# Kernel optimization log

Measured on AMD Instinct MI355X. Metric: run time of the kernel, lower is better.

## Reference

```python
import jax, jax.numpy as jnp
import numpy as np

D_MODEL = 1024
NHEAD = 16
HEAD_DIM = D_MODEL // NHEAD


def setup_inputs() -> dict:
    key = jax.random.key(0)
    ks = jax.random.split(key, 11)
    B, S = 2, 2048
    scale = 1.0 / np.sqrt(D_MODEL)
    inp = {
        "query": jax.random.normal(ks[0], (B, S, D_MODEL), jnp.float32),
        "key": jax.random.normal(ks[1], (B, S, D_MODEL), jnp.float32),
        "value": jax.random.normal(ks[2], (B, S, D_MODEL), jnp.float32),
        "Wq": jax.random.normal(ks[3], (D_MODEL, D_MODEL), jnp.float32) * scale,
        "bq": jnp.zeros((D_MODEL,), jnp.float32),
        "Wk": jax.random.normal(ks[4], (D_MODEL, D_MODEL), jnp.float32) * scale,
        "bk": jnp.zeros((D_MODEL,), jnp.float32),
        "Wv": jax.random.normal(ks[5], (D_MODEL, D_MODEL), jnp.float32) * scale,
        "bv": jnp.zeros((D_MODEL,), jnp.float32),
        "Wo": jax.random.normal(ks[6], (D_MODEL, D_MODEL), jnp.float32) * scale,
        "bo": jnp.zeros((D_MODEL,), jnp.float32),
    }
    return inp


def reference(query, key, value, Wq, bq, Wk, bk, Wv, bv, Wo, bo):
    B, S, _ = query.shape
    # Linear projections (torch Linear: x @ W.T + b)
    def proj(x, W, b):
        y = x @ W.T + b
        return y.reshape(B, -1, NHEAD, HEAD_DIM).transpose(0, 2, 1, 3)  # [B,H,S,hd]
    q = proj(query, Wq, bq)
    k = proj(key, Wk, bk)
    v = proj(value, Wv, bv)
    scores = jnp.einsum("bhqd,bhkd->bhqk", q, k) / np.sqrt(HEAD_DIM)
    attn = jax.nn.softmax(scores, axis=-1)  # dropout is identity (eval / p=0)
    out = jnp.einsum("bhqk,bhkd->bhqd", attn, v)
    out = out.transpose(0, 2, 1, 3).reshape(B, S, D_MODEL)
    return out @ Wo.T + bo
```

## Files before the change

### kernel.cpp

```cpp
#include <hip/hip_runtime.h>
#include <stdint.h>

typedef __attribute__((ext_vector_type(8))) short bf16x8;
typedef __attribute__((ext_vector_type(4))) short bf16x4;
typedef __attribute__((ext_vector_type(4))) float f32x4;
typedef __attribute__((ext_vector_type(2))) unsigned int u32x2;
typedef __attribute__((ext_vector_type(4))) unsigned int u32x4;
typedef unsigned int u32;
typedef unsigned short u16;

#define S_LEN 2048
#define DMODEL 1024
#define HD 64


static __device__ __forceinline__ u16 f2bf(float f) {
  u32 u = __builtin_bit_cast(u32, f);
  return (u16)((u + 0x7fffu + ((u >> 16) & 1u)) >> 16);
}

static __device__ __forceinline__ u32 cvt_pk(float a, float b) {
  u32 r;
  asm("v_cvt_pk_bf16_f32 %0, %1, %2" : "=v"(r) : "v"(a), "v"(b));
  return r;
}

static __device__ __forceinline__ void gl_lds16(const u16* g, u16* l) {
  __builtin_amdgcn_global_load_lds((const __attribute__((address_space(1))) u32*)g,
                                   (__attribute__((address_space(3))) u32*)l, 16, 0, 0);
}

static __device__ __forceinline__ u32 lds_addr(const void* p) {
  return (u32)(uint64_t)p;
}

static __device__ __forceinline__ bf16x4 tr16(u32 addr) {
  bf16x4 r;
  asm volatile("ds_read_b64_tr_b16 %0, %1" : "=v"(r) : "v"(addr));
  return r;
}

__global__ __launch_bounds__(256) void convert_w(
    const float* __restrict__ wq, const float* __restrict__ wk,
    const float* __restrict__ wv, const float* __restrict__ wo,
    u16* __restrict__ dst) {
  size_t i = ((size_t)blockIdx.x * 256 + threadIdx.x) * 8;
  u32 wsel = (u32)((i >> 20) & 3u);
  const float* src = (wsel == 0) ? wq : (wsel == 1) ? wk : (wsel == 2) ? wv : wo;
  size_t off = i & 0xFFFFFu;
  float4 a = *(const float4*)(src + off);
  float4 b = *(const float4*)(src + off + 4);
  bf16x8 o;
  o[0] = (short)f2bf(a.x); o[1] = (short)f2bf(a.y);
  o[2] = (short)f2bf(a.z); o[3] = (short)f2bf(a.w);
  o[4] = (short)f2bf(b.x); o[5] = (short)f2bf(b.y);
  o[6] = (short)f2bf(b.z); o[7] = (short)f2bf(b.w);
  *(bf16x8*)(dst + i) = o;
}

template <int OUT_BF16, int BN>
static __device__ __forceinline__ void gemm_core(
    const u16* __restrict__ A, const u16* __restrict__ Bm,
    const float* __restrict__ bias, void* __restrict__ Y, float scale,
    int bm, int bn, u16* As, u16* Bs) {
  const int tid = threadIdx.x;
  const int lane = tid & 63, w = tid >> 6;
  const int wm = w >> 1, wn = w & 1;
  const int g = lane >> 4, l15 = lane & 15;
  constexpr int NFR = BN / 64 * 2;

  f32x4 acc[4][NFR] = {};

  const int r0 = tid >> 2, k8 = (tid & 3) * 8;
  const int r1 = (tid + 256) >> 2;
  const size_t arow0 = (size_t)(bm * 128 + r0) * DMODEL + k8;
  const size_t arow1 = (size_t)(bm * 128 + r1) * DMODEL + k8;
  const size_t brow0 = (size_t)(bn * BN + r0) * DMODEL + k8;
  const size_t brow1 = (size_t)(bn * BN + r1) * DMODEL + k8;

  auto stage = [&](int buf, int kt) {
    const int kb = kt * 32;
    u16* asb = As + buf * 4096;
    u16* bsb = Bs + buf * (BN * 32);
    gl_lds16(A + arow0 + kb, asb + w * 512);
    gl_lds16(A + arow1 + kb, asb + w * 512 + 2048);
    gl_lds16(Bm + brow0 + kb, bsb + w * 512);
    if constexpr (BN == 128) gl_lds16(Bm + brow1 + kb, bsb + w * 512 + 2048);
  };

  stage(0, 0);
  __syncthreads();
  int cur = 0;
  for (int kt = 0; kt < 32; ++kt) {
    if (kt < 31) stage(cur ^ 1, kt + 1);
    const u16* as = As + cur * 4096;
    const u16* bs = Bs + cur * (BN * 32);
    bf16x8 a[4], b[NFR];
#pragma unroll
    for (int mi = 0; mi < 4; ++mi)
      a[mi] = *(const bf16x8*)&as[(wm * 64 + mi * 16 + l15) * 32 + g * 8];
#pragma unroll
    for (int ni = 0; ni < NFR; ++ni)
      b[ni] = *(const bf16x8*)&bs[(wn * (BN / 2) + ni * 16 + l15) * 32 + g * 8];
#pragma unroll
    for (int mi = 0; mi < 4; ++mi)
#pragma unroll
      for (int ni = 0; ni < NFR; ++ni)
        acc[mi][ni] = __builtin_amdgcn_mfma_f32_16x16x32_bf16(a[mi], b[ni], acc[mi][ni], 0, 0, 0);
    __syncthreads();
    cur ^= 1;
  }

#pragma unroll
  for (int ni = 0; ni < NFR; ++ni) {
    const int col = bn * BN + wn * (BN / 2) + ni * 16 + l15;
    const float bv = bias[col];
#pragma unroll
    for (int mi = 0; mi < 4; ++mi) {
      const int row0 = bm * 128 + wm * 64 + mi * 16 + g * 4;
#pragma unroll
      for (int r = 0; r < 4; ++r) {
        float v = (acc[mi][ni][r] + bv) * scale;
        if (OUT_BF16)
          ((u16*)Y)[(size_t)(row0 + r) * DMODEL + col] = f2bf(v);
        else
          ((float*)Y)[(size_t)(row0 + r) * DMODEL + col] = v;
      }
    }
  }
}

__global__ __launch_bounds__(512, 6) void qkv_gemm(
    const float* __restrict__ xq, const float* __restrict__ xk, const float* __restrict__ xv,
    const u16* __restrict__ W,
    const float* __restrict__ bq, const float* __restrict__ bk, const float* __restrict__ bv,
    u16* __restrict__ Qp, u16* __restrict__ Kpp, u16* __restrict__ Vpp, float qscale) {
  __shared__ u16 As[2 * 4096];
  __shared__ u16 Bs[2 * 4096];
  const int sel = blockIdx.x >> 8;
  const int bb = blockIdx.x & 255;
  const int bm = (bb & 7) * 4 + (bb >> 6);
  const int bn = (bb >> 3) & 7;
  const float* A = (sel == 0) ? xq : (sel == 1) ? xk : xv;
  const u16* Bm = W + (size_t)sel * (1024 * 1024);
  const float* bias = (sel == 0) ? bq : (sel == 1) ? bk : bv;
  u16* Y = (sel == 0) ? Qp : (sel == 1) ? Kpp : Vpp;
  const float scale = (sel == 0) ? qscale : 1.0f;

  const int tid = threadIdx.x;
  const int lane = tid & 63, w = tid >> 6;
  const int wm = w >> 2, wn = w & 3;
  const int g = lane >> 4, l15 = lane & 15;

  f32x4 acc[4][2] = {};

  const int r0 = tid >> 2, k8 = (tid & 3) * 8;
  const size_t arow0 = (size_t)(bm * 128 + r0) * DMODEL + k8;
  const size_t brow0 = (size_t)(bn * 128 + r0) * DMODEL + k8;

  float4 af0, af1;
  auto loadA = [&](int kt) {
    const int kb = kt * 32;
    af0 = *(const float4*)(A + arow0 + kb);
    af1 = *(const float4*)(A + arow0 + kb + 4);
  };
  auto writeA = [&](int buf) {
    u16* asb = As + buf * 4096;
    u32x4 p0 = {cvt_pk(af0.x, af0.y), cvt_pk(af0.z, af0.w),
                cvt_pk(af1.x, af1.y), cvt_pk(af1.z, af1.w)};
    *(u32x4*)(asb + tid * 8) = p0;
  };
  auto stageB = [&](int buf, int kt) {
    const int kb = kt * 32;
    u16* bsb = Bs + buf * 4096;
    gl_lds16(Bm + brow0 + kb, bsb + w * 512);
  };

  loadA(0);
  stageB(0, 0);
  writeA(0);
  __syncthreads();
  int cur = 0;
  for (int kt = 0; kt < 32; ++kt) {
    if (kt < 31) {
      loadA(kt + 1);
      stageB(cur ^ 1, kt + 1);
    }
    const u16* as = As + cur * 4096;
    const u16* bs = Bs + cur * 4096;
    bf16x8 a[4], b[2];
#pragma unroll
    for (int mi = 0; mi < 4; ++mi)
      a[mi] = *(const bf16x8*)&as[(wm * 64 + mi * 16 + l15) * 32 + g * 8];
#pragma unroll
    for (int ni = 0; ni < 2; ++ni)
      b[ni] = *(const bf16x8*)&bs[(wn * 32 + ni * 16 + l15) * 32 + g * 8];
#pragma unroll
    for (int mi = 0; mi < 4; ++mi)
#pragma unroll
      for (int ni = 0; ni < 2; ++ni)
        acc[mi][ni] = __builtin_amdgcn_mfma_f32_16x16x32_bf16(a[mi], b[ni], acc[mi][ni], 0, 0, 0);
    if (kt < 31) writeA(cur ^ 1);
    __syncthreads();
    cur ^= 1;
  }

#pragma unroll
  for (int ni = 0; ni < 2; ++ni) {
    const int col = bn * 128 + wn * 32 + ni * 16 + l15;
    const float bv = bias[col];
#pragma unroll
    for (int mi = 0; mi < 4; ++mi) {
      const int row0 = bm * 128 + wm * 64 + mi * 16 + g * 4;
#pragma unroll
      for (int r = 0; r < 4; ++r) {
        float v = (acc[mi][ni][r] + bv) * scale;
        ((u16*)Y)[(size_t)(row0 + r) * DMODEL + col] = f2bf(v);
      }
    }
  }
}

__global__ __launch_bounds__(256) void wo_gemm(
    const u16* __restrict__ A, const u16* __restrict__ Bm,
    const float* __restrict__ bias, float* __restrict__ Y) {
  __shared__ u16 As[2 * 4096];
  __shared__ u16 Bs[2 * 2048];
  const int idx = blockIdx.x;
  const int bm = (idx & 7) * 4 + (idx >> 7);
  const int bn = (idx >> 3) & 15;
  gemm_core<0, 64>(A, Bm, bias, Y, 1.0f, bm, bn, As, Bs);
}

__global__ __launch_bounds__(512, 4) void attn_fwd(
    const u16* __restrict__ Qp, const u16* __restrict__ Kp,
    const u16* __restrict__ Vp, u16* __restrict__ Op) {
  __shared__ u16 smem[32768];
  u16* Kl = smem;
  u16* Vl = smem + 8192;
  const int tid = threadIdx.x;
  const int lane = tid & 63, w = tid >> 6;
  const int g = lane >> 4, l15 = lane & 15;
  const int qs = w & 3, hf = w >> 2;
  const int xcd = blockIdx.x & 7;
  const int idx = blockIdx.x >> 3;
  const int bh = xcd * 4 + (idx >> 4);
  const int qt = idx & 15;
  const int b = bh >> 4, h = bh & 15;
  const size_t rowbase = (size_t)b * S_LEN;
  const int hcol = h * HD;

  bf16x8 qf[2][2];
#pragma unroll
  for (int qb = 0; qb < 2; ++qb) {
    const int qrow = qt * 128 + qs * 32 + qb * 16 + l15;
    qf[qb][0] = *(const bf16x8*)(Qp + (rowbase + qrow) * DMODEL + hcol + g * 8);
    qf[qb][1] = *(const bf16x8*)(Qp + (rowbase + qrow) * DMODEL + hcol + 32 + g * 8);
  }

  f32x4 o[2][4] = {};
  float lsum[2] = {0.0f, 0.0f};

  const u32 sbase = lds_addr(smem);

  const int half_s = tid >> 8;
  const int kvs = (tid >> 3) & 31, slot = (tid & 7) ^ (kvs & 7);
  const size_t koff = (rowbase + half_s * 1024 + kvs) * (size_t)DMODEL + hcol + slot * 8;
  const int cc = tid & 255;
  const int hh = cc & 1, p = (cc >> 1) & 15, sub = (cc >> 5) & 1, dt0 = (cc >> 6) & 3;
  const int kvv = 8 * (p >> 2) + sub * 4 + (p & 3);
  const size_t voff = (rowbase + half_s * 1024 + kvv) * (size_t)DMODEL + hcol + dt0 * 16 + hh * 8;

  auto stage = [&](int buf, int it) {
    const size_t adv = (size_t)it * 32 * DMODEL;
    gl_lds16(Kp + koff + adv, Kl + buf * 4096 + w * 512);
    gl_lds16(Vp + voff + adv, Vl + buf * 4096 + w * 512);
  };

  stage(0, 0);
  __syncthreads();
  int cur = 0;
  for (int it = 0; it < 32; ++it) {
    if (it < 31) stage(cur ^ 1, it + 1);
    const char* kb = (const char*)smem + cur * 8192 + hf * 4096;
    const u32 vbb = sbase + 16384 + (u32)(cur * 8192 + hf * 4096);
    const u32 pswz = (u32)((l15 & 7) << 4);

    f32x4 s[2][2];
    __builtin_amdgcn_s_setprio(1);
#pragma unroll
    for (int t = 0; t < 2; ++t) {
      const int kvl = t * 16 + l15;
      const u32 swz = (u32)((kvl & 7) << 4);
      bf16x8 k0 = *(const bf16x8*)(kb + (((u32)(kvl * 128 + g * 16)) ^ swz));
      bf16x8 k1 = *(const bf16x8*)(kb + (((u32)(kvl * 128 + 64 + g * 16)) ^ swz));
      f32x4 z = {};
      s[0][t] = __builtin_amdgcn_mfma_f32_16x16x32_bf16(
          k1, qf[0][1], __builtin_amdgcn_mfma_f32_16x16x32_bf16(k0, qf[0][0], z, 0, 0, 0), 0, 0, 0);
      s[1][t] = __builtin_amdgcn_mfma_f32_16x16x32_bf16(
          k1, qf[1][1], __builtin_amdgcn_mfma_f32_16x16x32_bf16(k0, qf[1][0], z, 0, 0, 0), 0, 0, 0);
    }
    __builtin_amdgcn_s_setprio(0);

#pragma unroll
    for (int qb = 0; qb < 2; ++qb) {
      const u32 pb = (u32)(32768 + (w * 2 + qb) * 2048 + l15 * 128);
      float psum = 0.0f;
#pragma unroll
      for (int t = 0; t < 2; ++t) {
        float e0 = __builtin_amdgcn_exp2f(s[qb][t][0]);
        float e1 = __builtin_amdgcn_exp2f(s[qb][t][1]);
        float e2 = __builtin_amdgcn_exp2f(s[qb][t][2]);
        float e3 = __builtin_amdgcn_exp2f(s[qb][t][3]);
        psum += (e0 + e1) + (e2 + e3);
        u32x2 pk = {cvt_pk(e0, e1), cvt_pk(e2, e3)};
        *(u32x2*)((char*)smem + ((pb + (u32)(t * 32 + g * 8)) ^ pswz)) = pk;
      }
      lsum[qb] += psum;
    }

    bf16x8 pf[2];
    bf16x4 tv[4][2];
#pragma unroll
    for (int qb = 0; qb < 2; ++qb) {
      const u32 pb = (u32)(32768 + (w * 2 + qb) * 2048 + l15 * 128);
      pf[qb] = *(const bf16x8*)((const char*)smem + ((pb + (u32)(g * 16)) ^ pswz));
    }
#pragma unroll
    for (int dt = 0; dt < 4; ++dt)
#pragma unroll
      for (int sb = 0; sb < 2; ++sb)
        tv[dt][sb] = tr16(vbb + (u32)((dt * 2 + sb) * 512 + lane * 8));
    asm volatile("s_waitcnt lgkmcnt(0)" ::: "memory");
    __builtin_amdgcn_sched_barrier(0);
    __builtin_amdgcn_s_setprio(1);
#pragma unroll
    for (int dt = 0; dt < 4; ++dt) {
      bf16x8 vf;
      vf[0] = tv[dt][0][0]; vf[1] = tv[dt][0][1];
      vf[2] = tv[dt][0][2]; vf[3] = tv[dt][0][3];
      vf[4] = tv[dt][1][0]; vf[5] = tv[dt][1][1];
      vf[6] = tv[dt][1][2]; vf[7] = tv[dt][1][3];
      o[0][dt] = __builtin_amdgcn_mfma_f32_16x16x32_bf16(pf[0], vf, o[0][dt], 0, 0, 0);
      o[1][dt] = __builtin_amdgcn_mfma_f32_16x16x32_bf16(pf[1], vf, o[1][dt], 0, 0, 0);
    }
    __builtin_amdgcn_s_setprio(0);
    __syncthreads();
    cur ^= 1;
  }

  float ls[2];
#pragma unroll
  for (int qb = 0; qb < 2; ++qb) {
    float v = lsum[qb];
    v += __shfl_xor(v, 16);
    v += __shfl_xor(v, 32);
    ls[qb] = v;
  }
  if (w >= 4) {
    char* ob = (char*)smem + (w - 4) * 8192 + lane * 16;
#pragma unroll
    for (int qb = 0; qb < 2; ++qb)
#pragma unroll
      for (int dt = 0; dt < 4; ++dt)
        *(f32x4*)(ob + (qb * 4 + dt) * 1024) = o[qb][dt];
    float2 lw = {ls[0], ls[1]};
    *(float2*)((char*)smem + 32768 + (w - 4) * 512 + lane * 8) = lw;
  }
  __syncthreads();
  if (w < 4) {
    const char* ob = (const char*)smem + w * 8192 + lane * 16;
#pragma unroll
    for (int qb = 0; qb < 2; ++qb)
#pragma unroll
      for (int dt = 0; dt < 4; ++dt)
        o[qb][dt] += *(const f32x4*)(ob + (qb * 4 + dt) * 1024);
    const float2 lp = *(const float2*)((const char*)smem + 32768 + w * 512 + lane * 8);
    ls[0] += lp.x;
    ls[1] += lp.y;
#pragma unroll
    for (int qb = 0; qb < 2; ++qb) {
      const float linv = 1.0f / ls[qb];
      const float li0 = __shfl(linv, g * 4 + 0);
      const float li1 = __shfl(linv, g * 4 + 1);
      const float li2 = __shfl(linv, g * 4 + 2);
      const float li3 = __shfl(linv, g * 4 + 3);
      const float li[4] = {li0, li1, li2, li3};
#pragma unroll
      for (int dt = 0; dt < 4; ++dt)
#pragma unroll
        for (int r = 0; r < 4; ++r) {
          const int qr = qt * 128 + w * 32 + qb * 16 + g * 4 + r;
          Op[(rowbase + qr) * DMODEL + hcol + dt * 16 + l15] = f2bf(o[qb][dt][r] * li[r]);
        }
    }
  }
}

extern "C" void kernel_launch(void* const* d_in, const int* in_sizes, int n_in,
                              void* d_out, int out_size, void* d_ws, size_t ws_size,
                              hipStream_t stream) {
  const float* xq = (const float*)d_in[0];
  const float* xk = (const float*)d_in[1];
  const float* xv = (const float*)d_in[2];
  const float* Wq = (const float*)d_in[3];
  const float* bq = (const float*)d_in[4];
  const float* Wk = (const float*)d_in[5];
  const float* bk = (const float*)d_in[6];
  const float* Wv = (const float*)d_in[7];
  const float* bv = (const float*)d_in[8];
  const float* Wo = (const float*)d_in[9];
  const float* bo = (const float*)d_in[10];

  u16* ws = (u16*)d_ws;
  const size_t MB4 = 4096ull * 1024ull;
  u16* WQb = ws + 3 * MB4;
  u16* Qp = ws + 4 * MB4;
  u16* Kpp = ws + 5 * MB4;
  u16* Vpp = ws + 6 * MB4;
  u16* Opp = ws + 7 * MB4;

  convert_w<<<2048, 256, 0, stream>>>(Wq, Wk, Wv, Wo, WQb);

  const float qscale = 0.125f * 1.44269504088896340736f;
  qkv_gemm<<<768, 512, 0, stream>>>(xq, xk, xv, WQb, bq, bk, bv, Qp, Kpp, Vpp, qscale);

  attn_fwd<<<512, 512, 0, stream>>>(Qp, Kpp, Vpp, Opp);

  wo_gemm<<<512, 256, 0, stream>>>(Opp, WQb + 3 * 1024 * 1024, bo, (float*)d_out);
}
```

Measured before the change: 113.5 us.

## Double K-tile depth in QKV GEMM and XOR-swizzle LDS layout

```diff
diff --git a/kernel.cpp b/kernel.cpp
--- a/kernel.cpp
+++ b/kernel.cpp
@@ -130,13 +130,13 @@
   }
 }
 
-__global__ __launch_bounds__(512, 6) void qkv_gemm(
+__global__ __launch_bounds__(512, 4) void qkv_gemm(
     const float* __restrict__ xq, const float* __restrict__ xk, const float* __restrict__ xv,
     const u16* __restrict__ W,
     const float* __restrict__ bq, const float* __restrict__ bk, const float* __restrict__ bv,
     u16* __restrict__ Qp, u16* __restrict__ Kpp, u16* __restrict__ Vpp, float qscale) {
-  __shared__ u16 As[2 * 4096];
-  __shared__ u16 Bs[2 * 4096];
+  __shared__ u16 As[2 * 8192];
+  __shared__ u16 Bs[2 * 8192];
   const int sel = blockIdx.x >> 8;
   const int bb = blockIdx.x & 255;
   const int bm = (bb & 7) * 4 + (bb >> 6);
@@ -154,26 +154,39 @@
 
   f32x4 acc[4][2] = {};
 
-  const int r0 = tid >> 2, k8 = (tid & 3) * 8;
-  const size_t arow0 = (size_t)(bm * 128 + r0) * DMODEL + k8;
-  const size_t brow0 = (size_t)(bn * 128 + r0) * DMODEL + k8;
-
-  float4 af0, af1;
+  const int r0 = tid >> 2, k16 = (tid & 3) * 16;
+  const size_t arow0 = (size_t)(bm * 128 + r0) * DMODEL + k16;
+  const int ua = 2 * (tid & 3);
+  const u32 adst0 = (u32)(r0 * 128 + ((ua ^ (r0 & 7)) << 4));
+  const u32 adst1 = (u32)(r0 * 128 + (((ua + 1) ^ (r0 & 7)) << 4));
+
+  const int br0 = tid >> 3, bu0 = (tid & 7) ^ (br0 & 7);
+  const int br1 = (tid + 512) >> 3, bu1 = (tid & 7) ^ (br1 & 7);
+  const size_t brow0 = (size_t)(bn * 128 + br0) * DMODEL + bu0 * 8;
+  const size_t brow1 = (size_t)(bn * 128 + br1) * DMODEL + bu1 * 8;
+
+  float4 af0, af1, af2, af3;
   auto loadA = [&](int kt) {
-    const int kb = kt * 32;
+    const int kb = kt * 64;
     af0 = *(const float4*)(A + arow0 + kb);
     af1 = *(const float4*)(A + arow0 + kb + 4);
+    af2 = *(const float4*)(A + arow0 + kb + 8);
+    af3 = *(const float4*)(A + arow0 + kb + 12);
   };
   auto writeA = [&](int buf) {
-    u16* asb = As + buf * 4096;
+    char* asb = (char*)(As + buf * 8192);
     u32x4 p0 = {cvt_pk(af0.x, af0.y), cvt_pk(af0.z, af0.w),
                 cvt_pk(af1.x, af1.y), cvt_pk(af1.z, af1.w)};
-    *(u32x4*)(asb + tid * 8) = p0;
+    u32x4 p1 = {cvt_pk(af2.x, af2.y), cvt_pk(af2.z, af2.w),
+                cvt_pk(af3.x, af3.y), cvt_pk(af3.z, af3.w)};
+    *(u32x4*)(asb + adst0) = p0;
+    *(u32x4*)(asb + adst1) = p1;
   };
   auto stageB = [&](int buf, int kt) {
-    const int kb = kt * 32;
-    u16* bsb = Bs + buf * 4096;
+    const int kb = kt * 64;
+    u16* bsb = Bs + buf * 8192;
     gl_lds16(Bm + brow0 + kb, bsb + w * 512);
+    gl_lds16(Bm + brow1 + kb, bsb + w * 512 + 4096);
   };
 
   loadA(0);
@@ -181,26 +194,35 @@
   writeA(0);
   __syncthreads();
   int cur = 0;
-  for (int kt = 0; kt < 32; ++kt) {
-    if (kt < 31) {
+  for (int kt = 0; kt < 16; ++kt) {
+    if (kt < 15) {
       loadA(kt + 1);
       stageB(cur ^ 1, kt + 1);
     }
-    const u16* as = As + cur * 4096;
-    const u16* bs = Bs + cur * 4096;
-    bf16x8 a[4], b[2];
-#pragma unroll
-    for (int mi = 0; mi < 4; ++mi)
-      a[mi] = *(const bf16x8*)&as[(wm * 64 + mi * 16 + l15) * 32 + g * 8];
-#pragma unroll
-    for (int ni = 0; ni < 2; ++ni)
-      b[ni] = *(const bf16x8*)&bs[(wn * 32 + ni * 16 + l15) * 32 + g * 8];
-#pragma unroll
-    for (int mi = 0; mi < 4; ++mi)
-#pragma unroll
-      for (int ni = 0; ni < 2; ++ni)
-        acc[mi][ni] = __builtin_amdgcn_mfma_f32_16x16x32_bf16(a[mi], b[ni], acc[mi][ni], 0, 0, 0);
-    if (kt < 31) writeA(cur ^ 1);
+    const char* as = (const char*)(As + cur * 8192);
+    const char* bs = (const char*)(Bs + cur * 8192);
+    bf16x8 a[2][4], b[2][2];
+#pragma unroll
+    for (int kk = 0; kk < 2; ++kk) {
+#pragma unroll
+      for (int mi = 0; mi < 4; ++mi) {
+        const int row = wm * 64 + mi * 16 + l15;
+        a[kk][mi] = *(const bf16x8*)(as + row * 128 + (((kk * 4 + g) ^ (row & 7)) << 4));
+      }
+#pragma unroll
+      for (int ni = 0; ni < 2; ++ni) {
+        const int row = wn * 32 + ni * 16 + l15;
+        b[kk][ni] = *(const bf16x8*)(bs + row * 128 + (((kk * 4 + g) ^ (row & 7)) << 4));
+      }
+    }
+#pragma unroll
+    for (int kk = 0; kk < 2; ++kk)
+#pragma unroll
+      for (int mi = 0; mi < 4; ++mi)
+#pragma unroll
+        for (int ni = 0; ni < 2; ++ni)
+          acc[mi][ni] = __builtin_amdgcn_mfma_f32_16x16x32_bf16(a[kk][mi], b[kk][ni], acc[mi][ni], 0, 0, 0);
+    if (kt < 15) writeA(cur ^ 1);
     __syncthreads();
     cur ^= 1;
   }
```

After: 127.7 us. 12.5% more time.
